# Performance work log

Hardware: AMD Instinct MI355X
Metric: run time of the kernel (lower is better)

The kernel has to match this reference:

```python
import jax, jax.numpy as jnp
import numpy as np

B, S, E, H, Dh = 2, 2048, 1024, 16, 64


def setup_inputs() -> dict:
    key = jax.random.key(0)
    ks = jax.random.split(key, 12)
    scale = 1.0 / np.sqrt(E)
    inp = {
        "query": jax.random.normal(ks[0], (B, S, E), jnp.float32),
        "key_": jax.random.normal(ks[1], (B, S, E), jnp.float32),
        "value": jax.random.normal(ks[2], (B, S, E), jnp.float32),
        # causal mask, broadcast over heads inside reference (mask==0 -> -inf)
        "mask": jnp.broadcast_to(jnp.tril(jnp.ones((S, S), jnp.int32)), (B, S, S)),
        "WQ": jax.random.normal(ks[3], (E, H * Dh), jnp.float32) * scale,
        "bQ": jnp.zeros((H * Dh,), jnp.float32),
        "WK": jax.random.normal(ks[4], (E, H * Dh), jnp.float32) * scale,
        "bK": jnp.zeros((H * Dh,), jnp.float32),
        "WV": jax.random.normal(ks[5], (E, H * Dh), jnp.float32) * scale,
        "bV": jnp.zeros((H * Dh,), jnp.float32),
        "WO": jax.random.normal(ks[6], (H * Dh, E), jnp.float32) * scale,
        "bO": jnp.zeros((E,), jnp.float32),
    }
    return inp


def reference(query, key_, value, mask, WQ, bQ, WK, bK, WV, bV, WO, bO):
    # projections -> [B, H, S, Dh]
    def proj(x, W, b):
        y = x @ W + b  # [B, S, H*Dh]
        return y.reshape(B, -1, H, Dh).transpose(0, 2, 1, 3)

    q = proj(query, WQ, bQ)
    k = proj(key_, WK, bK)
    v = proj(value, WV, bV)

    # scores [B, H, S, S]
    a = jnp.einsum("bhqd,bhkd->bhqk", q, k) / jnp.sqrt(jnp.float32(Dh))
    a = jnp.where(mask[:, None, :, :] == 0, -jnp.inf, a)
    alpha = jax.nn.softmax(a, axis=-1)
    z = jnp.einsum("bhqk,bhkd->bhqd", alpha, v)  # [B, H, S, Dh]
    z = z.transpose(0, 2, 1, 3).reshape(B, -1, H * Dh)
    return z @ WO + bO
```

## Files before the change

kernel.cpp:

```cpp
#include <hip/hip_runtime.h>
#include <hip/hip_bf16.h>
#include <math.h>

namespace {

constexpr int Bb = 2, Ss = 2048, Ee = 1024, Hh = 16, Dh = 64;
constexpr int M  = Bb * Ss;
constexpr int N  = Hh * Dh;
constexpr int Kd = Ee;

typedef __attribute__((ext_vector_type(8))) short bf16x8;
typedef __attribute__((ext_vector_type(4))) float f32x4;

__device__ inline unsigned short f2bf(float f) {
  return __builtin_bit_cast(unsigned short, __float2bfloat16(f));
}
__device__ inline unsigned pack2(float a, float b) {
  return (unsigned)f2bf(a) | ((unsigned)f2bf(b) << 16);
}
__device__ inline void load_lds16(const void* g, void* lds) {
  __builtin_amdgcn_global_load_lds((const __attribute__((address_space(1))) void*)g,
                                   (__attribute__((address_space(3))) void*)lds, 16, 0, 0);
}

__global__ __launch_bounds__(256) void convert3(const float* __restrict__ a0,
                                                const float* __restrict__ a1,
                                                const float* __restrict__ a2,
                                                unsigned short* __restrict__ o0,
                                                unsigned short* __restrict__ o1,
                                                unsigned short* __restrict__ o2) {
  const float* src = blockIdx.z == 0 ? a0 : (blockIdx.z == 1 ? a1 : a2);
  unsigned short* dst = blockIdx.z == 0 ? o0 : (blockIdx.z == 1 ? o1 : o2);
  size_t i = ((size_t)blockIdx.x * 256 + threadIdx.x) * 8;
  float4 u = ((const float4*)(src + i))[0];
  float4 v = ((const float4*)(src + i))[1];
  uint4 w;
  w.x = pack2(u.x, u.y);
  w.y = pack2(u.z, u.w);
  w.z = pack2(v.x, v.y);
  w.w = pack2(v.z, v.w);
  *((uint4*)(dst + i)) = w;
}

__global__ __launch_bounds__(256) void transposeW(const float* __restrict__ w0,
                                                  const float* __restrict__ w1,
                                                  const float* __restrict__ w2,
                                                  const float* __restrict__ w3,
                                                  unsigned short* __restrict__ t0,
                                                  unsigned short* __restrict__ t1,
                                                  unsigned short* __restrict__ t2,
                                                  unsigned short* __restrict__ t3) {
  const float* W = blockIdx.z == 0 ? w0 : (blockIdx.z == 1 ? w1 : (blockIdx.z == 2 ? w2 : w3));
  unsigned short* Wt = blockIdx.z == 0 ? t0 : (blockIdx.z == 1 ? t1 : (blockIdx.z == 2 ? t2 : t3));
  __shared__ float tl[32][33];
  const int t = threadIdx.x;
  const int r = t >> 5, c = t & 31;
  const int n0 = blockIdx.x * 32, k0 = blockIdx.y * 32;
#pragma unroll
  for (int i = 0; i < 4; ++i) tl[r + i * 8][c] = W[(size_t)(k0 + r + i * 8) * N + n0 + c];
  __syncthreads();
#pragma unroll
  for (int i = 0; i < 4; ++i) {
    int rr = r + i * 8;
    Wt[(size_t)(n0 + rr) * Kd + k0 + c] = f2bf(tl[c][rr]);
  }
}

__device__ __attribute__((always_inline)) inline void gemm_core(
    const unsigned short* __restrict__ A, const unsigned short* __restrict__ Wt,
    unsigned short* As0, unsigned short* As1, unsigned short* Bs0,
    unsigned short* Bs1, f32x4 (&acc)[4][4]) {
  const int t = threadIdx.x, l = t & 63, w = t >> 6;
  const int wr = w >> 1, wc = w & 1, lr = l & 15, kc = l >> 4;
  const int bm = blockIdx.y * 128, bn = blockIdx.x * 128;
  const int srow = t >> 2, sc4 = t & 3;
  const unsigned short* Ap1 = A + (size_t)(bm + srow) * Kd + sc4 * 8;
  const unsigned short* Ap2 = Ap1 + (size_t)64 * Kd;
  const unsigned short* Bp1 = Wt + (size_t)(bn + srow) * Kd + sc4 * 8;
  const unsigned short* Bp2 = Bp1 + (size_t)64 * Kd;
  const size_t d1 = (size_t)(w * 64) * 8, d2 = (size_t)(w * 64 + 256) * 8;

  auto stage = [&](unsigned short* Ab, unsigned short* Bb, int kk) {
    load_lds16(Ap1 + kk, Ab + d1);
    load_lds16(Ap2 + kk, Ab + d2);
    load_lds16(Bp1 + kk, Bb + d1);
    load_lds16(Bp2 + kk, Bb + d2);
  };
  auto compute = [&](const unsigned short* Ab, const unsigned short* Bb) {
    bf16x8 a[4], b[4];
#pragma unroll
    for (int m = 0; m < 4; ++m)
      a[m] = *(const bf16x8*)&Ab[(size_t)(wr * 64 + m * 16 + lr) * 32 + kc * 8];
#pragma unroll
    for (int n = 0; n < 4; ++n)
      b[n] = *(const bf16x8*)&Bb[(size_t)(wc * 64 + n * 16 + lr) * 32 + kc * 8];
#pragma unroll
    for (int m = 0; m < 4; ++m)
#pragma unroll
      for (int n = 0; n < 4; ++n)
        acc[m][n] = __builtin_amdgcn_mfma_f32_16x16x32_bf16(a[m], b[n], acc[m][n], 0, 0, 0);
  };

  stage(As0, Bs0, 0);
  __syncthreads();
  for (int kk = 0; kk < Kd; kk += 64) {
    if (kk + 32 < Kd) stage(As1, Bs1, kk + 32);
    compute(As0, Bs0);
    __syncthreads();
    if (kk + 64 < Kd) stage(As0, Bs0, kk + 64);
    compute(As1, Bs1);
    __syncthreads();
  }
}

__global__ __launch_bounds__(256) void qkv_gemm(
    const unsigned short* __restrict__ qb, const unsigned short* __restrict__ kb,
    const unsigned short* __restrict__ vb, const unsigned short* __restrict__ wqT,
    const unsigned short* __restrict__ wkT, const unsigned short* __restrict__ wvT,
    const float* __restrict__ bQ, const float* __restrict__ bK,
    const float* __restrict__ bV, unsigned short* __restrict__ Qw,
    unsigned short* __restrict__ Kw, unsigned short* __restrict__ Vt) {
  __shared__ alignas(16) unsigned short smem[4][128 * 32];
  const int z = blockIdx.z;
  const unsigned short* A  = z == 0 ? qb : (z == 1 ? kb : vb);
  const unsigned short* Wt = z == 0 ? wqT : (z == 1 ? wkT : wvT);
  const float* bias        = z == 0 ? bQ : (z == 1 ? bK : bV);

  f32x4 acc[4][4] = {};
  gemm_core(A, Wt, smem[0], smem[1], smem[2], smem[3], acc);

  const int t = threadIdx.x, l = t & 63, w = t >> 6;
  const int wr = w >> 1, wc = w & 1, lr = l & 15, kc = l >> 4;
  const int bm = blockIdx.y * 128, bn = blockIdx.x * 128;

  if (z <= 1) {
    unsigned short* Cout = z ? Kw : Qw;
    const float oscale = z ? 1.0f : 0.125f;
#pragma unroll
    for (int m = 0; m < 4; ++m)
#pragma unroll
      for (int n = 0; n < 4; ++n) {
        const int cg = bn + wc * 64 + n * 16 + lr;
        const float bv = bias[cg];
#pragma unroll
        for (int r = 0; r < 4; ++r) {
          const int rg = bm + wr * 64 + m * 16 + kc * 4 + r;
          const int b_ = rg >> 11, s = rg & (Ss - 1);
          const int h = cg >> 6, d = cg & 63;
          Cout[(((size_t)(b_ * Hh + h) * Ss + s) << 6) + d] =
              f2bf((acc[m][n][r] + bv) * oscale);
        }
      }
  } else {
    unsigned short(*Ct)[136] = reinterpret_cast<unsigned short(*)[136]>(&smem[0][0]);
    const int b_ = bm >> 11, sb = bm & (Ss - 1);
#pragma unroll
    for (int nh = 0; nh < 2; ++nh) {
      if (wc == nh) {
#pragma unroll
        for (int m = 0; m < 4; ++m)
#pragma unroll
          for (int n = 0; n < 4; ++n) {
            const int cg = bn + wc * 64 + n * 16 + lr;
            const float bv = bias[cg];
            const int cl = n * 16 + lr;
            const int s0 = wr * 64 + m * 16 + kc * 4;
            ushort4 pk;
            pk.x = f2bf(acc[m][n][0] + bv);
            pk.y = f2bf(acc[m][n][1] + bv);
            pk.z = f2bf(acc[m][n][2] + bv);
            pk.w = f2bf(acc[m][n][3] + bv);
            *(ushort4*)&Ct[cl][s0] = pk;
          }
      }
      __syncthreads();
#pragma unroll
      for (int i = 0; i < 4; ++i) {
        const int c = i * 256 + t;
        const int cl = c >> 4, ch = c & 15;
        const int cg = bn + nh * 64 + cl;
        const int h = cg >> 6, d = cg & 63;
        uint4 vv = *(const uint4*)&Ct[cl][ch * 8];
        *(uint4*)(Vt + (((size_t)(b_ * Hh + h) * Dh + d) << 11) + sb + ch * 8) = vv;
      }
      __syncthreads();
    }
  }
}

__global__ __launch_bounds__(256) void gemm_out(const unsigned short* __restrict__ A,
                                                const unsigned short* __restrict__ Wt,
                                                const float* __restrict__ bias,
                                                float* __restrict__ C) {
  __shared__ alignas(16) unsigned short smem[4][128 * 32];
  f32x4 acc[4][4] = {};
  gemm_core(A, Wt, smem[0], smem[1], smem[2], smem[3], acc);

  const int t = threadIdx.x, l = t & 63, w = t >> 6;
  const int wr = w >> 1, wc = w & 1, lr = l & 15, kc = l >> 4;
  const int bm = blockIdx.y * 128, bn = blockIdx.x * 128;
#pragma unroll
  for (int m = 0; m < 4; ++m)
#pragma unroll
    for (int n = 0; n < 4; ++n) {
      const int cg = bn + wc * 64 + n * 16 + lr;
      const float bv = bias[cg];
#pragma unroll
      for (int r = 0; r < 4; ++r) {
        const int rg = bm + wr * 64 + m * 16 + kc * 4 + r;
        C[(size_t)rg * N + cg] = acc[m][n][r] + bv;
      }
    }
}

__global__ __launch_bounds__(256) void attn_mfma(const unsigned short* __restrict__ Q,
                                                 const unsigned short* __restrict__ K,
                                                 const unsigned short* __restrict__ Vt,
                                                 unsigned short* __restrict__ Z) {
  __shared__ alignas(16) unsigned short Ks[64 * 64];
  __shared__ alignas(16) unsigned short Vs[64 * 64];
  __shared__ alignas(16) unsigned short Ps[4][16 * 64];

  const int bh = blockIdx.x;
  const int qt = blockIdx.y;
  const int b  = bh >> 4, h = bh & 15;
  const int t  = threadIdx.x;
  const int l  = t & 63;
  const int w  = t >> 6;
  const int lr = l & 15;
  const int lg = l >> 4;

  const int qrow = qt * 64 + w * 16 + lr;
  const unsigned short* Qp = Q + ((size_t)bh * Ss + qrow) * Dh;
  bf16x8 bq[2];
  bq[0] = *(const bf16x8*)(Qp + lg * 8);
  bq[1] = *(const bf16x8*)(Qp + 32 + lg * 8);

  f32x4 o[4] = {};
  float mrow = -INFINITY, lsum = 0.f;

  const int srow = l >> 3;
  const int scol = ((l & 7) ^ srow) * 16;
  const char* Kg = (const char*)(K + (size_t)bh * Ss * Dh);
  const char* Vg = (const char*)(Vt + (size_t)bh * Dh * Ss);
  unsigned short* kD0 = Ks + (w * 16) * 64;
  unsigned short* kD1 = Ks + (w * 16 + 8) * 64;
  unsigned short* vD0 = Vs + (w * 16) * 64;
  unsigned short* vD1 = Vs + (w * 16 + 8) * 64;
  const char* vr0 = Vg + (size_t)(w * 16 + srow) * (Ss * 2) + scol;
  const char* vr1 = Vg + (size_t)(w * 16 + 8 + srow) * (Ss * 2) + scol;

  const int rx = (lr & 7) << 4;

  const int kv_tiles = qt + 1;
  for (int kt = 0; kt < kv_tiles; ++kt) {
    const int kv0 = kt * 64;
    __syncthreads();
    load_lds16(Kg + (size_t)(kv0 + w * 16 + srow) * 128 + scol, kD0);
    load_lds16(Kg + (size_t)(kv0 + w * 16 + 8 + srow) * 128 + scol, kD1);
    load_lds16(vr0 + kv0 * 2, vD0);
    load_lds16(vr1 + kv0 * 2, vD1);
    __syncthreads();

    f32x4 sa[4];
#pragma unroll
    for (int f = 0; f < 4; ++f) {
      sa[f] = (f32x4){0.f, 0.f, 0.f, 0.f};
#pragma unroll
      for (int kk = 0; kk < 2; ++kk) {
        const int cb = (kk * 64 + lg * 16) ^ rx;
        bf16x8 ak = *(const bf16x8*)((const char*)Ks + (f * 16 + lr) * 128 + cb);
        sa[f] = __builtin_amdgcn_mfma_f32_16x16x32_bf16(ak, bq[kk], sa[f], 0, 0, 0);
      }
    }

    if (kt == kv_tiles - 1) {
#pragma unroll
      for (int f = 0; f < 4; ++f)
#pragma unroll
        for (int r = 0; r < 4; ++r) {
          const int kg = kv0 + f * 16 + lg * 4 + r;
          if (kg > qrow) sa[f][r] = -INFINITY;
        }
    }

    float pmax = sa[0][0];
#pragma unroll
    for (int f = 0; f < 4; ++f)
#pragma unroll
      for (int r = 0; r < 4; ++r) pmax = fmaxf(pmax, sa[f][r]);
    pmax = fmaxf(pmax, __shfl_xor(pmax, 16));
    pmax = fmaxf(pmax, __shfl_xor(pmax, 32));
    const float mnew = fmaxf(mrow, pmax);
    const float sc   = __expf(mrow - mnew);

    float p[4][4];
    float psum = 0.f;
#pragma unroll
    for (int f = 0; f < 4; ++f)
#pragma unroll
      for (int r = 0; r < 4; ++r) {
        p[f][r] = __expf(sa[f][r] - mnew);
        psum += p[f][r];
      }
    psum += __shfl_xor(psum, 16);
    psum += __shfl_xor(psum, 32);
    lsum = lsum * sc + psum;
    mrow = mnew;

    float scr[4];
#pragma unroll
    for (int r = 0; r < 4; ++r) scr[r] = __shfl(sc, lg * 4 + r);
#pragma unroll
    for (int n = 0; n < 4; ++n)
#pragma unroll
      for (int r = 0; r < 4; ++r) o[n][r] *= scr[r];

    {
      char* Pw = (char*)Ps[w] + lr * 128;
#pragma unroll
      for (int f = 0; f < 4; ++f) {
        const int k0b = f * 32 + lg * 8;
        *(unsigned*)(Pw + ((k0b) ^ rx))     = pack2(p[f][0], p[f][1]);
        *(unsigned*)(Pw + ((k0b + 4) ^ rx)) = pack2(p[f][2], p[f][3]);
      }
    }

#pragma unroll
    for (int kk = 0; kk < 2; ++kk) {
      const int cb = (kk * 64 + lg * 16) ^ rx;
      bf16x8 ap = *(const bf16x8*)((const char*)Ps[w] + lr * 128 + cb);
#pragma unroll
      for (int n = 0; n < 4; ++n) {
        bf16x8 bv = *(const bf16x8*)((const char*)Vs + (n * 16 + lr) * 128 + cb);
        o[n] = __builtin_amdgcn_mfma_f32_16x16x32_bf16(ap, bv, o[n], 0, 0, 0);
      }
    }
  }

  const float linv = 1.f / lsum;
  float li[4];
#pragma unroll
  for (int r = 0; r < 4; ++r) li[r] = __shfl(linv, lg * 4 + r);
#pragma unroll
  for (int n = 0; n < 4; ++n)
#pragma unroll
    for (int r = 0; r < 4; ++r) {
      const int qg = qt * 64 + w * 16 + lg * 4 + r;
      Z[((size_t)(b * Ss + qg)) * N + h * 64 + n * 16 + lr] =
          f2bf(o[n][r] * li[r]);
    }
}

}

extern "C" void kernel_launch(void* const* d_in, const int* in_sizes, int n_in,
                              void* d_out, int out_size, void* d_ws, size_t ws_size,
                              hipStream_t stream) {
  const float* query = (const float*)d_in[0];
  const float* key_  = (const float*)d_in[1];
  const float* value = (const float*)d_in[2];
  const float* WQ = (const float*)d_in[4];
  const float* bQ = (const float*)d_in[5];
  const float* WK = (const float*)d_in[6];
  const float* bK = (const float*)d_in[7];
  const float* WV = (const float*)d_in[8];
  const float* bV = (const float*)d_in[9];
  const float* WO = (const float*)d_in[10];
  const float* bO = (const float*)d_in[11];
  float* out = (float*)d_out;

  const size_t mat = (size_t)M * N;
  unsigned short* qb  = (unsigned short*)d_ws;
  unsigned short* kb  = qb + mat;
  unsigned short* vb  = kb + mat;
  unsigned short* wqT = vb + mat;
  unsigned short* wkT = wqT + (size_t)N * Kd;
  unsigned short* wvT = wkT + (size_t)N * Kd;
  unsigned short* woT = wvT + (size_t)N * Kd;
  unsigned short* Qw  = woT + (size_t)N * Kd;
  unsigned short* Kw  = Qw + mat;
  unsigned short* Vw  = Kw + mat;
  unsigned short* zb  = qb;

  convert3<<<dim3(mat / 2048, 1, 3), 256, 0, stream>>>(query, key_, value, qb, kb, vb);
  transposeW<<<dim3(N / 32, Kd / 32, 4), 256, 0, stream>>>(WQ, WK, WV, WO, wqT, wkT, wvT, woT);

  qkv_gemm<<<dim3(N / 128, M / 128, 3), 256, 0, stream>>>(qb, kb, vb, wqT, wkT, wvT,
                                                          bQ, bK, bV, Qw, Kw, Vw);

  attn_mfma<<<dim3(Bb * Hh, Ss / 64), 256, 0, stream>>>(Qw, Kw, Vw, zb);

  gemm_out<<<dim3(N / 128, M / 128), 256, 0, stream>>>(zb, woT, bO, out);
}
```

Before: 267.5 us.

## Pair mirrored causal query tiles per block and skip redundant rescaling

Each attention block now handles two query tiles, qt and its mirror (31-qt), so every block does the same amount of causal work. The two tiles share each K/V tile loaded into LDS, which halves the grid and cuts repeated K/V loads. It also adds a lazy online-softmax rescale that only updates the running max when it grows by more than 8, and sets wave priority around the MFMA sections. In exchange, each block runs longer and uses more registers, and there are half as many blocks to fill the GPU.

```diff
diff --git a/kernel.cpp b/kernel.cpp
--- a/kernel.cpp
+++ b/kernel.cpp
@@ -221,8 +221,9 @@
   __shared__ alignas(16) unsigned short Vs[64 * 64];
   __shared__ alignas(16) unsigned short Ps[4][16 * 64];
 
-  const int bh = blockIdx.x;
-  const int qt = blockIdx.y;
+  const int bh  = blockIdx.x;
+  const int qtA = blockIdx.y;
+  const int qtB = (Ss / 64 - 1) - qtA;
   const int b  = bh >> 4, h = bh & 15;
   const int t  = threadIdx.x;
   const int l  = t & 63;
@@ -230,14 +231,18 @@
   const int lr = l & 15;
   const int lg = l >> 4;
 
-  const int qrow = qt * 64 + w * 16 + lr;
-  const unsigned short* Qp = Q + ((size_t)bh * Ss + qrow) * Dh;
-  bf16x8 bq[2];
-  bq[0] = *(const bf16x8*)(Qp + lg * 8);
-  bq[1] = *(const bf16x8*)(Qp + 32 + lg * 8);
-
-  f32x4 o[4] = {};
-  float mrow = -INFINITY, lsum = 0.f;
+  const int qrowA = qtA * 64 + w * 16 + lr;
+  const int qrowB = qtB * 64 + w * 16 + lr;
+  const unsigned short* QpA = Q + ((size_t)bh * Ss + qrowA) * Dh;
+  const unsigned short* QpB = Q + ((size_t)bh * Ss + qrowB) * Dh;
+  bf16x8 bqA[2], bqB[2];
+  bqA[0] = *(const bf16x8*)(QpA + lg * 8);
+  bqA[1] = *(const bf16x8*)(QpA + 32 + lg * 8);
+  bqB[0] = *(const bf16x8*)(QpB + lg * 8);
+  bqB[1] = *(const bf16x8*)(QpB + 32 + lg * 8);
+
+  f32x4 oA[4] = {}, oB[4] = {};
+  float mA = -INFINITY, lA = 0.f, mB = -INFINITY, lB = 0.f;
 
   const int srow = l >> 3;
   const int scol = ((l & 7) ^ srow) * 16;
@@ -252,8 +257,92 @@
 
   const int rx = (lr & 7) << 4;
 
-  const int kv_tiles = qt + 1;
-  for (int kt = 0; kt < kv_tiles; ++kt) {
+  auto process = [&](const bf16x8 (&bq)[2], f32x4 (&o)[4], float& mrow,
+                     float& lsum, int qrow, bool diag, int kv0) {
+    f32x4 sa[4];
+    __builtin_amdgcn_s_setprio(1);
+#pragma unroll
+    for (int f = 0; f < 4; ++f) {
+      sa[f] = (f32x4){0.f, 0.f, 0.f, 0.f};
+#pragma unroll
+      for (int kk = 0; kk < 2; ++kk) {
+        const int cb = (kk * 64 + lg * 16) ^ rx;
+        bf16x8 ak = *(const bf16x8*)((const char*)Ks + (f * 16 + lr) * 128 + cb);
+        sa[f] = __builtin_amdgcn_mfma_f32_16x16x32_bf16(ak, bq[kk], sa[f], 0, 0, 0);
+      }
+    }
+    __builtin_amdgcn_s_setprio(0);
+
+    if (diag) {
+#pragma unroll
+      for (int f = 0; f < 4; ++f)
+#pragma unroll
+        for (int r = 0; r < 4; ++r) {
+          const int kg = kv0 + f * 16 + lg * 4 + r;
+          if (kg > qrow) sa[f][r] = -INFINITY;
+        }
+    }
+
+    float pmax = sa[0][0];
+#pragma unroll
+    for (int f = 0; f < 4; ++f)
+#pragma unroll
+      for (int r = 0; r < 4; ++r) pmax = fmaxf(pmax, sa[f][r]);
+    pmax = fmaxf(pmax, __shfl_xor(pmax, 16));
+    pmax = fmaxf(pmax, __shfl_xor(pmax, 32));
+
+    if (!__all(pmax <= mrow + 8.f)) {
+      const float mnew = fmaxf(mrow, pmax);
+      const float sc = __expf(mrow - mnew);
+      lsum *= sc;
+      float scr[4];
+#pragma unroll
+      for (int r = 0; r < 4; ++r) scr[r] = __shfl(sc, lg * 4 + r);
+#pragma unroll
+      for (int n = 0; n < 4; ++n)
+#pragma unroll
+        for (int r = 0; r < 4; ++r) o[n][r] *= scr[r];
+      mrow = mnew;
+    }
+
+    float p[4][4];
+    float psum = 0.f;
+#pragma unroll
+    for (int f = 0; f < 4; ++f)
+#pragma unroll
+      for (int r = 0; r < 4; ++r) {
+        p[f][r] = __expf(sa[f][r] - mrow);
+        psum += p[f][r];
+      }
+    psum += __shfl_xor(psum, 16);
+    psum += __shfl_xor(psum, 32);
+    lsum += psum;
+
+    {
+      char* Pw = (char*)Ps[w] + lr * 128;
+#pragma unroll
+      for (int f = 0; f < 4; ++f) {
+        const int k0b = f * 32 + lg * 8;
+        *(unsigned*)(Pw + ((k0b) ^ rx))     = pack2(p[f][0], p[f][1]);
+        *(unsigned*)(Pw + ((k0b + 4) ^ rx)) = pack2(p[f][2], p[f][3]);
+      }
+    }
+
+    __builtin_amdgcn_s_setprio(1);
+#pragma unroll
+    for (int kk = 0; kk < 2; ++kk) {
+      const int cb = (kk * 64 + lg * 16) ^ rx;
+      bf16x8 ap = *(const bf16x8*)((const char*)Ps[w] + lr * 128 + cb);
+#pragma unroll
+      for (int n = 0; n < 4; ++n) {
+        bf16x8 bv = *(const bf16x8*)((const char*)Vs + (n * 16 + lr) * 128 + cb);
+        o[n] = __builtin_amdgcn_mfma_f32_16x16x32_bf16(ap, bv, o[n], 0, 0, 0);
+      }
+    }
+    __builtin_amdgcn_s_setprio(0);
+  };
+
+  for (int kt = 0; kt <= qtB; ++kt) {
     const int kv0 = kt * 64;
     __syncthreads();
     load_lds16(Kg + (size_t)(kv0 + w * 16 + srow) * 128 + scol, kD0);
@@ -262,94 +351,26 @@
     load_lds16(vr1 + kv0 * 2, vD1);
     __syncthreads();
 
-    f32x4 sa[4];
-#pragma unroll
-    for (int f = 0; f < 4; ++f) {
-      sa[f] = (f32x4){0.f, 0.f, 0.f, 0.f};
-#pragma unroll
-      for (int kk = 0; kk < 2; ++kk) {
-        const int cb = (kk * 64 + lg * 16) ^ rx;
-        bf16x8 ak = *(const bf16x8*)((const char*)Ks + (f * 16 + lr) * 128 + cb);
-        sa[f] = __builtin_amdgcn_mfma_f32_16x16x32_bf16(ak, bq[kk], sa[f], 0, 0, 0);
-      }
-    }
-
-    if (kt == kv_tiles - 1) {
-#pragma unroll
-      for (int f = 0; f < 4; ++f)
-#pragma unroll
-        for (int r = 0; r < 4; ++r) {
-          const int kg = kv0 + f * 16 + lg * 4 + r;
-          if (kg > qrow) sa[f][r] = -INFINITY;
-        }
-    }
-
-    float pmax = sa[0][0];
-#pragma unroll
-    for (int f = 0; f < 4; ++f)
-#pragma unroll
-      for (int r = 0; r < 4; ++r) pmax = fmaxf(pmax, sa[f][r]);
-    pmax = fmaxf(pmax, __shfl_xor(pmax, 16));
-    pmax = fmaxf(pmax, __shfl_xor(pmax, 32));
-    const float mnew = fmaxf(mrow, pmax);
-    const float sc   = __expf(mrow - mnew);
-
-    float p[4][4];
-    float psum = 0.f;
-#pragma unroll
-    for (int f = 0; f < 4; ++f)
+    process(bqB, oB, mB, lB, qrowB, kt == qtB, kv0);
+    if (kt <= qtA) process(bqA, oA, mA, lA, qrowA, kt == qtA, kv0);
+  }
+
+  auto epilogue = [&](f32x4 (&o)[4], float lsum, int qt) {
+    const float linv = 1.f / lsum;
+    float li[4];
+#pragma unroll
+    for (int r = 0; r < 4; ++r) li[r] = __shfl(linv, lg * 4 + r);
+#pragma unroll
+    for (int n = 0; n < 4; ++n)
 #pragma unroll
       for (int r = 0; r < 4; ++r) {
-        p[f][r] = __expf(sa[f][r] - mnew);
-        psum += p[f][r];
-      }
-    psum += __shfl_xor(psum, 16);
-    psum += __shfl_xor(psum, 32);
-    lsum = lsum * sc + psum;
-    mrow = mnew;
-
-    float scr[4];
-#pragma unroll
-    for (int r = 0; r < 4; ++r) scr[r] = __shfl(sc, lg * 4 + r);
-#pragma unroll
-    for (int n = 0; n < 4; ++n)
-#pragma unroll
-      for (int r = 0; r < 4; ++r) o[n][r] *= scr[r];
-
-    {
-      char* Pw = (char*)Ps[w] + lr * 128;
-#pragma unroll
-      for (int f = 0; f < 4; ++f) {
-        const int k0b = f * 32 + lg * 8;
-        *(unsigned*)(Pw + ((k0b) ^ rx))     = pack2(p[f][0], p[f][1]);
-        *(unsigned*)(Pw + ((k0b + 4) ^ rx)) = pack2(p[f][2], p[f][3]);
-      }
-    }
-
-#pragma unroll
-    for (int kk = 0; kk < 2; ++kk) {
-      const int cb = (kk * 64 + lg * 16) ^ rx;
-      bf16x8 ap = *(const bf16x8*)((const char*)Ps[w] + lr * 128 + cb);
-#pragma unroll
-      for (int n = 0; n < 4; ++n) {
-        bf16x8 bv = *(const bf16x8*)((const char*)Vs + (n * 16 + lr) * 128 + cb);
-        o[n] = __builtin_amdgcn_mfma_f32_16x16x32_bf16(ap, bv, o[n], 0, 0, 0);
-      }
-    }
-  }
-
-  const float linv = 1.f / lsum;
-  float li[4];
-#pragma unroll
-  for (int r = 0; r < 4; ++r) li[r] = __shfl(linv, lg * 4 + r);
-#pragma unroll
-  for (int n = 0; n < 4; ++n)
-#pragma unroll
-    for (int r = 0; r < 4; ++r) {
-      const int qg = qt * 64 + w * 16 + lg * 4 + r;
-      Z[((size_t)(b * Ss + qg)) * N + h * 64 + n * 16 + lr] =
-          f2bf(o[n][r] * li[r]);
-    }
+        const int qg = qt * 64 + w * 16 + lg * 4 + r;
+        Z[((size_t)(b * Ss + qg)) * N + h * 64 + n * 16 + lr] =
+            f2bf(o[n][r] * li[r]);
+      }
+  };
+  epilogue(oA, lA, qtA);
+  epilogue(oB, lB, qtB);
 }
 
 }
@@ -389,7 +410,7 @@
   qkv_gemm<<<dim3(N / 128, M / 128, 3), 256, 0, stream>>>(qb, kb, vb, wqT, wkT, wvT,
                                                           bQ, bK, bV, Qw, Kw, Vw);
 
-  attn_mfma<<<dim3(Bb * Hh, Ss / 64), 256, 0, stream>>>(Qw, Kw, Vw, zb);
+  attn_mfma<<<dim3(Bb * Hh, Ss / 128), 256, 0, stream>>>(Qw, Kw, Vw, zb);
 
   gemm_out<<<dim3(N / 128, M / 128), 256, 0, stream>>>(zb, woT, bO, out);
 }
```

Result: faster. 255.3 us (-4.6%).
